# Optimization experiments

Measured on AMD Instinct MI355X. Metric: run time of the kernel, lower is better.

Reference implementation:

```python
import jax, jax.numpy as jnp
import numpy as np
from jax import lax

B, M = 8192, 200
OUT_W = OUT_H = 16
NUM_LAYERS = 32
CNN_CH = 64
FLAT = CNN_CH * 2 * 2  # conv5/s3: 16->4, conv3/s1: 4->2
INPUT_SIZE = 128
HIDDEN = 128
CRITIC_H = 1024
ACTOR_H = 512
EMB_D = 16
NUM_ACTIONS = 100


def setup_inputs() -> dict:
    key = jax.random.key(0)
    ks = jax.random.split(key, 20)
    # token observations: [coord_byte, attr_index, attr_value] packed as int32
    coords = jax.random.randint(ks[0], (B, M), 0, 256)          # coord byte; 255 = invalid token
    attrs = jax.random.randint(ks[1], (B, M), 0, 40)            # some >= NUM_LAYERS -> masked
    vals = jax.random.randint(ks[2], (B, M), 0, 256)
    observations = jnp.stack([coords, attrs, vals], axis=-1).astype(jnp.int32)

    def lin(k, out_d, in_d, scale=None):
        s = scale if scale is not None else 1.0 / np.sqrt(in_d)
        return jax.random.uniform(k, (out_d, in_d), jnp.float32, -s, s)

    max_vec = jax.random.uniform(ks[3], (1, NUM_LAYERS, 1, 1), jnp.float32, 0.5, 30.0)
    cnn1_w = jax.random.normal(ks[4], (CNN_CH, NUM_LAYERS, 5, 5), jnp.float32) * 0.05
    cnn1_b = jnp.zeros((CNN_CH,), jnp.float32)
    cnn2_w = jax.random.normal(ks[5], (CNN_CH, CNN_CH, 3, 3), jnp.float32) * 0.05
    cnn2_b = jnp.zeros((CNN_CH,), jnp.float32)
    fc1_w = lin(ks[6], 128, FLAT); fc1_b = jnp.zeros((128,), jnp.float32)
    enc_w = lin(ks[7], INPUT_SIZE, 128); enc_b = jnp.zeros((INPUT_SIZE,), jnp.float32)
    critic1_w = lin(ks[8], CRITIC_H, HIDDEN); critic1_b = jnp.zeros((CRITIC_H,), jnp.float32)
    value_w = lin(ks[9], 1, CRITIC_H); value_b = jnp.zeros((1,), jnp.float32)
    actor1_w = lin(ks[10], ACTOR_H, HIDDEN); actor1_b = jnp.zeros((ACTOR_H,), jnp.float32)
    emb = jax.random.normal(ks[11], (NUM_ACTIONS, EMB_D), jnp.float32)
    action_emb = emb * (0.1 / jnp.max(jnp.abs(emb)))
    bound = 1.0 / np.sqrt(ACTOR_H)
    actor_W = jax.random.uniform(ks[12], (1, ACTOR_H, EMB_D), jnp.float32, -bound, bound)
    actor_bias = jax.random.uniform(ks[13], (1,), jnp.float32, -bound, bound)
    return dict(observations=observations, max_vec=max_vec,
                cnn1_w=cnn1_w, cnn1_b=cnn1_b, cnn2_w=cnn2_w, cnn2_b=cnn2_b,
                fc1_w=fc1_w, fc1_b=fc1_b, enc_w=enc_w, enc_b=enc_b,
                critic1_w=critic1_w, critic1_b=critic1_b, value_w=value_w, value_b=value_b,
                actor1_w=actor1_w, actor1_b=actor1_b, action_emb=action_emb,
                actor_W=actor_W, actor_bias=actor_bias)


def _encode_box(observations):
    # bit-unpack coord byte, mask, scatter into dense [B, L, W, H] box
    coords = observations[..., 0]                       # [B, M]
    x_idx = (coords >> 4) & 15
    y_idx = coords & 15
    atr_idx = observations[..., 1]
    atr_val = observations[..., 2].astype(jnp.float32)
    valid = (coords != 255) & (atr_idx < NUM_LAYERS)
    dim = OUT_W * OUT_H
    combined = atr_idx * dim + x_idx * OUT_H + y_idx    # [B, M]
    safe_idx = jnp.where(valid, combined, 0)
    safe_val = jnp.where(valid, atr_val, 0.0)
    box = jnp.zeros((observations.shape[0], NUM_LAYERS * dim), jnp.float32)
    box = box.at[jnp.arange(observations.shape[0])[:, None], safe_idx].set(safe_val)
    return box.reshape(-1, NUM_LAYERS, OUT_W, OUT_H)


def _conv(x, w, b, stride):
    y = lax.conv_general_dilated(x, w, (stride, stride), 'VALID',
                                 dimension_numbers=('NCHW', 'OIHW', 'NCHW'))
    return y + b[None, :, None, None]


def reference(observations, max_vec, cnn1_w, cnn1_b, cnn2_w, cnn2_b, fc1_w, fc1_b,
              enc_w, enc_b, critic1_w, critic1_b, value_w, value_b,
              actor1_w, actor1_b, action_emb, actor_W, actor_bias):
    box = _encode_box(observations)
    x = box / max_vec
    x = jax.nn.relu(_conv(x, cnn1_w, cnn1_b, 3))
    x = jax.nn.relu(_conv(x, cnn2_w, cnn2_b, 1))
    x = x.reshape(x.shape[0], -1)                       # [B, FLAT]
    x = jax.nn.relu(x @ fc1_w.T + fc1_b)
    hidden = jax.nn.relu(x @ enc_w.T + enc_b)           # [B, 128]
    # critic
    cf = jnp.tanh(hidden @ critic1_w.T + critic1_b)
    value = cf @ value_w.T + value_b                    # [B, 1]
    # bilinear actor (k=1: query is action-independent)
    af = jax.nn.relu(hidden @ actor1_w.T + actor1_b)    # [B, ACTOR_H]
    query = jnp.tanh(jnp.einsum('bh,he->be', af, actor_W[0]))
    logits = query @ action_emb[:NUM_ACTIONS].T + actor_bias  # [B, NUM_ACTIONS]
    return logits, value
```

## Files before the change

kernel.cpp:

```cpp
#include <hip/hip_runtime.h>
#include <math.h>

#define B_ 8192

typedef __attribute__((ext_vector_type(8))) short short8;
typedef __attribute__((ext_vector_type(4))) float f32x4;

__device__ unsigned short g_w1p[51200];
__device__ unsigned short g_w2p[36864];
__device__ unsigned short g_fc1hi[32768], g_fc1lo[32768];
__device__ unsigned short g_enchi[16384], g_enclo[16384];
__device__ unsigned short g_crp[131072];
__device__ unsigned short g_acp[65536];
__device__ unsigned short g_qWp[8192];
__device__ unsigned short g_ACT1hi[8192*1024];

__device__ __forceinline__ unsigned short f2bf(float v){
    unsigned u = __builtin_bit_cast(unsigned, v);
    unsigned r = (u + 0x7fffu + ((u >> 16) & 1u)) >> 16;
    return (unsigned short)r;
}
__device__ __forceinline__ float bf2f(unsigned short h){
    unsigned u = ((unsigned)h) << 16;
    return __builtin_bit_cast(float, u);
}
__device__ __forceinline__ void split_store(float v, unsigned short* hi, unsigned short* lo){
    unsigned short h = f2bf(v);
    *hi = h;
    *lo = f2bf(v - bf2f(h));
}

__global__ __launch_bounds__(256) void prep_kernel(
    const float* __restrict__ w1, const float* __restrict__ maxv,
    const float* __restrict__ w2, const float* __restrict__ fc1,
    const float* __restrict__ enc, const float* __restrict__ cr,
    const float* __restrict__ ac, const float* __restrict__ aW)
{
    int d = blockIdx.x * 256 + threadIdx.x;
    if (d < 51200){
        int n = d / 800, k = d - n*800;
        int l = k / 25;
        float v = w1[d] / maxv[l];
        int kc = k >> 5, kh = k & 31, ng = n >> 4, r = n & 15;
        int idx = ((kc*4 + ng)*16 + r)*32 + kh;
        g_w1p[idx] = f2bf(v);
        return;
    }
    d -= 51200;
    if (d < 36864){
        int oc = d / 576, k2 = d - oc*576;
        int kxy = k2 >> 6, ic = k2 & 63;
        float v = w2[oc*576 + ic*9 + kxy];
        int kc = k2 >> 6, ks = (k2 >> 5) & 1, kq = k2 & 31, nt = oc >> 4, r = oc & 15;
        int idx = (((kc*2 + ks)*4 + nt)*16 + r)*32 + kq;
        g_w2p[idx] = f2bf(v);
        return;
    }
    d -= 36864;
    if (d < 32768){
        int n = d >> 8, kp = d & 255;
        float v = fc1[n*256 + (kp & 63)*4 + (kp >> 6)];
        int idx = ((((n >> 4)*8) + (kp >> 5))*16 + (n & 15))*32 + (kp & 31);
        split_store(v, &g_fc1hi[idx], &g_fc1lo[idx]);
        return;
    }
    d -= 32768;
    if (d < 16384){
        int n = d >> 7, k = d & 127;
        int idx = ((((n >> 4)*4) + (k >> 5))*16 + (n & 15))*32 + (k & 31);
        split_store(enc[d], &g_enchi[idx], &g_enclo[idx]);
        return;
    }
    d -= 16384;
    if (d < 131072){
        int n = d >> 7, k = d & 127;
        int idx = ((((n >> 4)*4) + (k >> 5))*16 + (n & 15))*32 + (k & 31);
        g_crp[idx] = f2bf(cr[d]);
        return;
    }
    d -= 131072;
    if (d < 65536){
        int n = d >> 7, k = d & 127;
        int idx = ((((n >> 4)*4) + (k >> 5))*16 + (n & 15))*32 + (k & 31);
        g_acp[idx] = f2bf(ac[d]);
        return;
    }
    d -= 65536;
    {
        int e = d >> 9, j = d & 511;
        int idx = ((j >> 5)*16 + e)*32 + (j & 31);
        g_qWp[idx] = f2bf(aW[j*16 + e]);
    }
}

#define APITCH2 424
__global__ __launch_bounds__(256, 5) void conv1_kernel(const int* __restrict__ obs,
                                                       const float* __restrict__ b1)
{
    const int b = blockIdx.x;
    const int tid = threadIdx.x;
    const int wave = tid >> 6, lane = tid & 63;
    const int l15 = lane & 15, lhi = lane >> 4;

    __shared__ int wtab[8192];
    unsigned short* sA = (unsigned short*)wtab;

    int   cells[2], xs[2], ys[2], ls[2];
    float vals[2];
    bool  valids[2], kept[2];
    #pragma unroll
    for (int u = 0; u < 2; u++){
        const int slot = tid + u*256;
        valids[u] = false; kept[u] = false; cells[u] = 0;
        if (slot < 400){
            const int si = (slot >= 200) ? 1 : 0;
            const int k  = slot - si*200;
            const int base = (b*2 + si)*600 + k*3;
            int coord = obs[base], atr = obs[base+1], val = obs[base+2];
            bool valid = (coord != 255) && (atr < 32);
            xs[u] = (coord >> 4) & 15;  ys[u] = coord & 15;  ls[u] = atr;
            cells[u] = valid ? (atr*256 + xs[u]*16 + ys[u]) : 0;
            vals[u]  = (float)val;
            valids[u] = valid;
        }
    }
    if (tid < 200) wtab[cells[0]] = -1;
    __syncthreads();
    if (tid < 200) atomicMax(&wtab[cells[0]], tid);
    __syncthreads();
    if (tid < 200) kept[0] = (wtab[cells[0]] == tid);
    __syncthreads();
    if (tid >= 200) wtab[cells[0]] = -1;
    if (tid < 144)  wtab[cells[1]] = -1;
    __syncthreads();
    if (tid >= 200) atomicMax(&wtab[cells[0]], tid - 200);
    if (tid < 144)  atomicMax(&wtab[cells[1]], tid + 56);
    __syncthreads();
    if (tid >= 200) kept[0] = (wtab[cells[0]] == tid - 200);
    if (tid < 144)  kept[1] = (wtab[cells[1]] == tid + 56);
    __syncthreads();

    f32x4 acc0e = {0,0,0,0}, acc1e = {0,0,0,0};
    f32x4 acc0o = {0,0,0,0}, acc1o = {0,0,0,0};
    const unsigned short* Bhp = &g_w1p[wave*512 + l15*32 + lhi*8];
    const unsigned short* A0 = &sA[l15*APITCH2 + lhi*8];
    const unsigned short* A1 = &sA[(16 + l15)*APITCH2 + lhi*8];

    #pragma unroll
    for (int pass = 0; pass < 2; pass++){
        for (int i = tid; i < 1696; i += 256)
            *(short8*)&sA[i * 8] = short8{0,0,0,0,0,0,0,0};
        __syncthreads();

        #pragma unroll
        for (int u = 0; u < 2; u++){
            const int slot = tid + u*256;
            if (slot < 400 && kept[u] && valids[u]){
                const int si = (slot >= 200) ? 1 : 0;
                const int x3 = xs[u]/3, rx = xs[u] - 3*x3;
                const int y3 = ys[u]/3, ry = ys[u] - 3*y3;
                const unsigned short hv = f2bf(vals[u]);
                #pragma unroll
                for (int d = 0; d < 4; d++){
                    const int dxd = d >> 1, dyd = d & 1;
                    const int ox = x3 - dxd, oy = y3 - dyd;
                    const int wx = rx + 3*dxd, wy = ry + 3*dyd;
                    if (((unsigned)ox <= 3u) && ((unsigned)oy <= 3u) && (wx < 5) && (wy < 5)){
                        const int c = ls[u]*25 + wx*5 + wy;
                        const bool inpass = (pass == 0) ? (c < 416) : (c >= 416);
                        if (inpass)
                            sA[(si*16 + ox*4 + oy)*APITCH2 + (c - pass*416)] = hv;
                    }
                }
            }
        }
        __syncthreads();

        const int kc0 = (pass == 0) ? 0 : 13;
        const int kc1 = (pass == 0) ? 13 : 25;
        #pragma unroll
        for (int kc = kc0; kc < kc1; kc++){
            const int kl = kc - kc0;
            short8 a0 = *(const short8*)&A0[kl*32];
            short8 a1 = *(const short8*)&A1[kl*32];
            const short8 bb8 = *(const short8*)&Bhp[kc*2048];
            if (kc & 1){
                acc0o = __builtin_amdgcn_mfma_f32_16x16x32_bf16(a0, bb8, acc0o, 0, 0, 0);
                acc1o = __builtin_amdgcn_mfma_f32_16x16x32_bf16(a1, bb8, acc1o, 0, 0, 0);
            } else {
                acc0e = __builtin_amdgcn_mfma_f32_16x16x32_bf16(a0, bb8, acc0e, 0, 0, 0);
                acc1e = __builtin_amdgcn_mfma_f32_16x16x32_bf16(a1, bb8, acc1e, 0, 0, 0);
            }
        }
        if (pass == 0) __syncthreads();
    }

    f32x4 acc0, acc1;
    #pragma unroll
    for (int j = 0; j < 4; j++){ acc0[j] = acc0e[j] + acc0o[j]; acc1[j] = acc1e[j] + acc1o[j]; }

    const int n = wave*16 + l15;
    const float bb = b1[n];
    #pragma unroll
    for (int j = 0; j < 4; j++){
        const int pos = lhi*4 + j;
        float v0 = fmaxf(acc0[j] + bb, 0.f);
        float v1 = fmaxf(acc1[j] + bb, 0.f);
        g_ACT1hi[(b*2    )*1024 + pos*64 + n] = f2bf(v0);
        g_ACT1hi[(b*2 + 1)*1024 + pos*64 + n] = f2bf(v1);
    }
}

__global__ __launch_bounds__(512, 4) void tail_kernel(
    const float* __restrict__ b2,   const float* __restrict__ fc1b,
    const float* __restrict__ encb, const float* __restrict__ crb,
    const float* __restrict__ vw,   const float* __restrict__ vb,
    const float* __restrict__ acb,  const float* __restrict__ emb,
    const float* __restrict__ abias, float* __restrict__ out)
{
    const int r0 = blockIdx.x * 16;
    const int tid = threadIdx.x, wave = tid >> 6, lane = tid & 63;
    const int l15 = lane & 15, lhi = lane >> 4;
    const int coff = l15*32 + lhi*8;

    __shared__ char smem[52736];
    unsigned short* sA1h = (unsigned short*)smem;
    unsigned short* sA1l = (unsigned short*)(smem + 8448);
    float*          qpart= (float*)smem;
    unsigned short* sXh  = (unsigned short*)(smem + 16896);
    unsigned short* sXl  = (unsigned short*)(smem + 21248);
    float* svred = (float*)(smem + 16896);
    float* sq    = (float*)(smem + 17408);
    float* semb  = (float*)(smem + 18496);
    unsigned short* sHh  = (unsigned short*)(smem + 25600);
    unsigned short* sHl  = (unsigned short*)(smem + 29952);
    unsigned short* cb   = (unsigned short*)(smem + 34304);
    unsigned short* sACT = (unsigned short*)(smem + 16896);

    {
        for (int u = tid; u < 2048; u += 512){
            const int row = u >> 7, c8 = (u & 127) * 8;
            *(short8*)&sACT[row*1032 + c8] = *(const short8*)&g_ACT1hi[(r0 + row)*1024 + c8];
        }
        __syncthreads();

        f32x4 c2acc[2] = {{0,0,0,0},{0,0,0,0}};
        const int tile0 = wave*2,     mt0 = tile0 >> 2, nt0 = tile0 & 3;
        const int tile1 = wave*2 + 1, mt1 = tile1 >> 2, nt1 = tile1 & 3;
        const int row0 = mt0*16 + l15, smp0 = row0 >> 2, px0 = (row0 >> 1) & 1, py0 = row0 & 1;
        const int row1 = mt1*16 + l15, smp1 = row1 >> 2, px1 = (row1 >> 1) & 1, py1 = row1 & 1;
        #pragma unroll
        for (int kc = 0; kc < 9; kc++){
            const int kx = kc / 3, ky = kc - 3*kx;
            const int cell0 = (px0 + kx)*4 + (py0 + ky);
            const int cell1 = (px1 + kx)*4 + (py1 + ky);
            #pragma unroll
            for (int ks = 0; ks < 2; ks++){
                const int kk = ks*32 + lhi*8;
                short8 a0 = *(const short8*)&sACT[smp0*1032 + cell0*64 + kk];
                short8 a1 = *(const short8*)&sACT[smp1*1032 + cell1*64 + kk];
                const short8 b0 = *(const short8*)&g_w2p[((kc*2 + ks)*4 + nt0)*512 + coff];
                const short8 b1 = *(const short8*)&g_w2p[((kc*2 + ks)*4 + nt1)*512 + coff];
                c2acc[0] = __builtin_amdgcn_mfma_f32_16x16x32_bf16(a0, b0, c2acc[0], 0, 0, 0);
                c2acc[1] = __builtin_amdgcn_mfma_f32_16x16x32_bf16(a1, b1, c2acc[1], 0, 0, 0);
            }
        }
        __syncthreads();
        #pragma unroll
        for (int wt = 0; wt < 2; wt++){
            const int tile = wave*2 + wt, mt = tile >> 2, nt = tile & 3;
            const int col = nt*16 + l15;
            const float bb = b2[col];
            #pragma unroll
            for (int j = 0; j < 4; j++){
                const int row = mt*16 + lhi*4 + j;
                float v = fmaxf(c2acc[wt][j] + bb, 0.f);
                unsigned short h = f2bf(v);
                const int ai = (row >> 2)*264 + (row & 3)*64 + col;
                sA1h[ai] = h;
                sA1l[ai] = f2bf(v - bf2f(h));
            }
        }
    }
    __syncthreads();

    {
        f32x4 acc = {0,0,0,0};
        const int n = wave*16 + l15;
        #pragma unroll
        for (int kk8 = 0; kk8 < 8; kk8++){
            const int kk = kk8*32 + lhi*8;
            short8 ah = *(const short8*)&sA1h[l15*264 + kk];
            short8 al = *(const short8*)&sA1l[l15*264 + kk];
            const short8 bh = *(const short8*)&g_fc1hi[(wave*8 + kk8)*512 + coff];
            const short8 bl = *(const short8*)&g_fc1lo[(wave*8 + kk8)*512 + coff];
            acc = __builtin_amdgcn_mfma_f32_16x16x32_bf16(ah, bh, acc, 0, 0, 0);
            acc = __builtin_amdgcn_mfma_f32_16x16x32_bf16(al, bh, acc, 0, 0, 0);
            acc = __builtin_amdgcn_mfma_f32_16x16x32_bf16(ah, bl, acc, 0, 0, 0);
        }
        __syncthreads();
        const float bb = fc1b[n];
        #pragma unroll
        for (int j = 0; j < 4; j++){
            const int row = lhi*4 + j;
            float v = fmaxf(acc[j] + bb, 0.f);
            unsigned short h = f2bf(v);
            sXh[row*136 + n] = h;
            sXl[row*136 + n] = f2bf(v - bf2f(h));
        }
    }
    __syncthreads();

    {
        f32x4 acc = {0,0,0,0};
        const int n = wave*16 + l15;
        #pragma unroll
        for (int kk4 = 0; kk4 < 4; kk4++){
            const int kk = kk4*32 + lhi*8;
            short8 ah = *(const short8*)&sXh[l15*136 + kk];
            short8 al = *(const short8*)&sXl[l15*136 + kk];
            const short8 bh = *(const short8*)&g_enchi[(wave*4 + kk4)*512 + coff];
            const short8 bl = *(const short8*)&g_enclo[(wave*4 + kk4)*512 + coff];
            acc = __builtin_amdgcn_mfma_f32_16x16x32_bf16(ah, bh, acc, 0, 0, 0);
            acc = __builtin_amdgcn_mfma_f32_16x16x32_bf16(al, bh, acc, 0, 0, 0);
            acc = __builtin_amdgcn_mfma_f32_16x16x32_bf16(ah, bl, acc, 0, 0, 0);
        }
        const float bb = encb[n];
        #pragma unroll
        for (int j = 0; j < 4; j++){
            const int row = lhi*4 + j;
            float v = fmaxf(acc[j] + bb, 0.f);
            unsigned short h = f2bf(v);
            sHh[row*136 + n] = h;
            sHl[row*136 + n] = f2bf(v - bf2f(h));
        }
    }
    __syncthreads();

    short8 Ah[4], Al[4];
    #pragma unroll
    for (int kk4 = 0; kk4 < 4; kk4++){
        const int kk = kk4*32 + lhi*8;
        Ah[kk4] = *(const short8*)&sHh[l15*136 + kk];
        Al[kk4] = *(const short8*)&sHl[l15*136 + kk];
    }

    {
        float vp[4] = {0,0,0,0};
        #pragma unroll
        for (int ntc = 0; ntc < 2; ntc++){
            f32x4 cacc[4];
            #pragma unroll
            for (int q = 0; q < 4; q++) cacc[q] = f32x4{0,0,0,0};
            #pragma unroll
            for (int q = 0; q < 4; q++){
                const int t = wave*8 + ntc*4 + q;
                #pragma unroll
                for (int kk4 = 0; kk4 < 4; kk4++){
                    const short8 bh = *(const short8*)&g_crp[(t*4 + kk4)*512 + coff];
                    cacc[q] = __builtin_amdgcn_mfma_f32_16x16x32_bf16(Ah[kk4], bh, cacc[q], 0, 0, 0);
                    cacc[q] = __builtin_amdgcn_mfma_f32_16x16x32_bf16(Al[kk4], bh, cacc[q], 0, 0, 0);
                }
            }
            #pragma unroll
            for (int q = 0; q < 4; q++){
                const int n = wave*128 + (ntc*4 + q)*16 + l15;
                const float w = vw[n], bb = crb[n];
                #pragma unroll
                for (int j = 0; j < 4; j++)
                    vp[j] += tanhf(cacc[q][j] + bb) * w;
            }
        }
        #pragma unroll
        for (int m = 1; m < 16; m <<= 1)
            #pragma unroll
            for (int j = 0; j < 4; j++) vp[j] += __shfl_xor(vp[j], m, 64);
        if (l15 == 0){
            #pragma unroll
            for (int j = 0; j < 4; j++)
                svred[wave*16 + lhi*4 + j] = vp[j];
        }
    }

    __syncthreads();
    f32x4 qacc = {0,0,0,0};
    {
        const int c = wave;
        f32x4 aacc[4];
        #pragma unroll
        for (int nt = 0; nt < 4; nt++) aacc[nt] = f32x4{0,0,0,0};
        #pragma unroll
        for (int kk4 = 0; kk4 < 4; kk4++){
            #pragma unroll
            for (int nt = 0; nt < 4; nt++){
                const int t = c*4 + nt;
                const short8 bh = *(const short8*)&g_acp[(t*4 + kk4)*512 + coff];
                aacc[nt] = __builtin_amdgcn_mfma_f32_16x16x32_bf16(Ah[kk4], bh, aacc[nt], 0, 0, 0);
                aacc[nt] = __builtin_amdgcn_mfma_f32_16x16x32_bf16(Al[kk4], bh, aacc[nt], 0, 0, 0);
            }
        }
        #pragma unroll
        for (int nt = 0; nt < 4; nt++){
            const int col = nt*16 + l15;
            const float bb = acb[c*64 + col];
            #pragma unroll
            for (int j = 0; j < 4; j++){
                const int row = lhi*4 + j;
                cb[(wave*16 + row)*72 + col] = f2bf(fmaxf(aacc[nt][j] + bb, 0.f));
            }
        }
        #pragma unroll
        for (int kk2 = 0; kk2 < 2; kk2++){
            const int kk = kk2*32 + lhi*8;
            const short8 qbh = *(const short8*)&g_qWp[(c*2 + kk2)*512 + coff];
            const short8 qah = *(const short8*)&cb[(wave*16 + l15)*72 + kk];
            qacc = __builtin_amdgcn_mfma_f32_16x16x32_bf16(qah, qbh, qacc, 0, 0, 0);
        }
    }
    #pragma unroll
    for (int j = 0; j < 4; j++)
        qpart[wave*256 + (lhi*4 + j)*16 + l15] = qacc[j];
    __syncthreads();

    if (tid < 16){
        float s = vb[0];
        #pragma unroll
        for (int w = 0; w < 8; w++) s += svred[w*16 + tid];
        out[B_*100 + r0 + tid] = s;
    }
    if (tid < 256){
        int row = tid >> 4, e = tid & 15;
        float s = 0.f;
        #pragma unroll
        for (int w = 0; w < 8; w++) s += qpart[w*256 + row*16 + e];
        sq[row*17 + e] = tanhf(s);
    }
    for (int k = tid; k < 1600; k += 512) semb[k] = emb[k];
    __syncthreads();
    for (int i = tid; i < 1600; i += 512){
        int row = i / 100, a = i - row*100;
        float s = abias[0];
        #pragma unroll
        for (int e = 0; e < 16; e++) s += sq[row*17 + e] * semb[a*16 + e];
        out[(r0 + row)*100 + a] = s;
    }
}

extern "C" void kernel_launch(void* const* d_in, const int* in_sizes, int n_in,
                              void* d_out, int out_size, void* d_ws, size_t ws_size,
                              hipStream_t stream) {
    const int*   obs   = (const int*)  d_in[0];
    const float* maxv  = (const float*)d_in[1];
    const float* w1    = (const float*)d_in[2];
    const float* b1    = (const float*)d_in[3];
    const float* w2    = (const float*)d_in[4];
    const float* b2    = (const float*)d_in[5];
    const float* fc1w  = (const float*)d_in[6];
    const float* fc1b  = (const float*)d_in[7];
    const float* encw  = (const float*)d_in[8];
    const float* encb  = (const float*)d_in[9];
    const float* crw   = (const float*)d_in[10];
    const float* crb   = (const float*)d_in[11];
    const float* vw    = (const float*)d_in[12];
    const float* vb    = (const float*)d_in[13];
    const float* acw   = (const float*)d_in[14];
    const float* acb   = (const float*)d_in[15];
    const float* emb   = (const float*)d_in[16];
    const float* aW    = (const float*)d_in[17];
    const float* abias = (const float*)d_in[18];
    float* out = (float*)d_out;

    prep_kernel<<<1336, 256, 0, stream>>>(w1, maxv, w2, fc1w, encw, crw, acw, aW);
    conv1_kernel<<<B_/2, 256, 0, stream>>>(obs, b1);
    tail_kernel<<<512, 512, 0, stream>>>(b2, fc1b, encb, crb, vw, vb, acb, emb, abias, out);
}
```

Measured before the change: 82.59 us.

## Process four samples per conv1 block to reuse weight loads across more MFMAs

Each conv1 block now handles four batch samples instead of two, so each B-fragment load of the conv weights feeds four MFMAs instead of two, and half as many blocks are launched. The dedup of tokens is serialised per sample over four rounds with barriers, the shared A tile doubles to 64 rows, and the even/odd accumulator split is dropped. Occupancy hint drops from 5 to 3 blocks per CU, and the extra barriers plus the larger zero-fill may offset the gain in weight reuse.

```diff
diff --git a/kernel.cpp b/kernel.cpp
--- a/kernel.cpp
+++ b/kernel.cpp
@@ -93,8 +93,8 @@
     }
 }
 
-#define APITCH2 424
-__global__ __launch_bounds__(256, 5) void conv1_kernel(const int* __restrict__ obs,
+#define APITCH4 424
+__global__ __launch_bounds__(256, 3) void conv1_kernel(const int* __restrict__ obs,
                                                        const float* __restrict__ b1)
 {
     const int b = blockIdx.x;
@@ -102,61 +102,58 @@
     const int wave = tid >> 6, lane = tid & 63;
     const int l15 = lane & 15, lhi = lane >> 4;
 
-    __shared__ int wtab[8192];
-    unsigned short* sA = (unsigned short*)wtab;
-
-    int   cells[2], xs[2], ys[2], ls[2];
-    float vals[2];
-    bool  valids[2], kept[2];
-    #pragma unroll
-    for (int u = 0; u < 2; u++){
+    __shared__ char smem[64 * APITCH4 * 2];
+    int* wtab = (int*)smem;
+    unsigned short* sA = (unsigned short*)smem;
+
+    int   cells[4], xs[4], ys[4], ls[4], ks[4], sis[4];
+    float vals[4];
+    bool  valids[4], kept[4], act[4];
+    #pragma unroll
+    for (int u = 0; u < 4; u++){
         const int slot = tid + u*256;
-        valids[u] = false; kept[u] = false; cells[u] = 0;
-        if (slot < 400){
-            const int si = (slot >= 200) ? 1 : 0;
+        act[u] = (slot < 800);
+        valids[u] = false; kept[u] = false; cells[u] = 0; sis[u] = 0; ks[u] = 0;
+        if (act[u]){
+            const int si = slot / 200;
             const int k  = slot - si*200;
-            const int base = (b*2 + si)*600 + k*3;
+            const int base = (b*4 + si)*600 + k*3;
             int coord = obs[base], atr = obs[base+1], val = obs[base+2];
             bool valid = (coord != 255) && (atr < 32);
             xs[u] = (coord >> 4) & 15;  ys[u] = coord & 15;  ls[u] = atr;
             cells[u] = valid ? (atr*256 + xs[u]*16 + ys[u]) : 0;
             vals[u]  = (float)val;
-            valids[u] = valid;
-        }
-    }
-    if (tid < 200) wtab[cells[0]] = -1;
-    __syncthreads();
-    if (tid < 200) atomicMax(&wtab[cells[0]], tid);
-    __syncthreads();
-    if (tid < 200) kept[0] = (wtab[cells[0]] == tid);
-    __syncthreads();
-    if (tid >= 200) wtab[cells[0]] = -1;
-    if (tid < 144)  wtab[cells[1]] = -1;
-    __syncthreads();
-    if (tid >= 200) atomicMax(&wtab[cells[0]], tid - 200);
-    if (tid < 144)  atomicMax(&wtab[cells[1]], tid + 56);
-    __syncthreads();
-    if (tid >= 200) kept[0] = (wtab[cells[0]] == tid - 200);
-    if (tid < 144)  kept[1] = (wtab[cells[1]] == tid + 56);
-    __syncthreads();
-
-    f32x4 acc0e = {0,0,0,0}, acc1e = {0,0,0,0};
-    f32x4 acc0o = {0,0,0,0}, acc1o = {0,0,0,0};
+            valids[u] = valid; sis[u] = si; ks[u] = k;
+        }
+    }
+    #pragma unroll
+    for (int s = 0; s < 4; s++){
+        #pragma unroll
+        for (int u = 0; u < 4; u++)
+            if (act[u] && sis[u] == s) wtab[cells[u]] = -1;
+        __syncthreads();
+        #pragma unroll
+        for (int u = 0; u < 4; u++)
+            if (act[u] && sis[u] == s) atomicMax(&wtab[cells[u]], ks[u]);
+        __syncthreads();
+        #pragma unroll
+        for (int u = 0; u < 4; u++)
+            if (act[u] && sis[u] == s) kept[u] = (wtab[cells[u]] == ks[u]);
+        __syncthreads();
+    }
+
+    f32x4 acc[4] = {{0,0,0,0},{0,0,0,0},{0,0,0,0},{0,0,0,0}};
     const unsigned short* Bhp = &g_w1p[wave*512 + l15*32 + lhi*8];
-    const unsigned short* A0 = &sA[l15*APITCH2 + lhi*8];
-    const unsigned short* A1 = &sA[(16 + l15)*APITCH2 + lhi*8];
 
     #pragma unroll
     for (int pass = 0; pass < 2; pass++){
-        for (int i = tid; i < 1696; i += 256)
+        for (int i = tid; i < 3392; i += 256)
             *(short8*)&sA[i * 8] = short8{0,0,0,0,0,0,0,0};
         __syncthreads();
 
         #pragma unroll
-        for (int u = 0; u < 2; u++){
-            const int slot = tid + u*256;
-            if (slot < 400 && kept[u] && valids[u]){
-                const int si = (slot >= 200) ? 1 : 0;
+        for (int u = 0; u < 4; u++){
+            if (act[u] && kept[u] && valids[u]){
                 const int x3 = xs[u]/3, rx = xs[u] - 3*x3;
                 const int y3 = ys[u]/3, ry = ys[u] - 3*y3;
                 const unsigned short hv = f2bf(vals[u]);
@@ -169,7 +166,7 @@
                         const int c = ls[u]*25 + wx*5 + wy;
                         const bool inpass = (pass == 0) ? (c < 416) : (c >= 416);
                         if (inpass)
-                            sA[(si*16 + ox*4 + oy)*APITCH2 + (c - pass*416)] = hv;
+                            sA[(sis[u]*16 + ox*4 + oy)*APITCH4 + (c - pass*416)] = hv;
                     }
                 }
             }
@@ -181,33 +178,26 @@
         #pragma unroll
         for (int kc = kc0; kc < kc1; kc++){
             const int kl = kc - kc0;
-            short8 a0 = *(const short8*)&A0[kl*32];
-            short8 a1 = *(const short8*)&A1[kl*32];
             const short8 bb8 = *(const short8*)&Bhp[kc*2048];
-            if (kc & 1){
-                acc0o = __builtin_amdgcn_mfma_f32_16x16x32_bf16(a0, bb8, acc0o, 0, 0, 0);
-                acc1o = __builtin_amdgcn_mfma_f32_16x16x32_bf16(a1, bb8, acc1o, 0, 0, 0);
-            } else {
-                acc0e = __builtin_amdgcn_mfma_f32_16x16x32_bf16(a0, bb8, acc0e, 0, 0, 0);
-                acc1e = __builtin_amdgcn_mfma_f32_16x16x32_bf16(a1, bb8, acc1e, 0, 0, 0);
+            #pragma unroll
+            for (int m = 0; m < 4; m++){
+                short8 am = *(const short8*)&sA[(m*16 + l15)*APITCH4 + kl*32 + lhi*8];
+                acc[m] = __builtin_amdgcn_mfma_f32_16x16x32_bf16(am, bb8, acc[m], 0, 0, 0);
             }
         }
         if (pass == 0) __syncthreads();
     }
-
-    f32x4 acc0, acc1;
-    #pragma unroll
-    for (int j = 0; j < 4; j++){ acc0[j] = acc0e[j] + acc0o[j]; acc1[j] = acc1e[j] + acc1o[j]; }
 
     const int n = wave*16 + l15;
     const float bb = b1[n];
     #pragma unroll
-    for (int j = 0; j < 4; j++){
-        const int pos = lhi*4 + j;
-        float v0 = fmaxf(acc0[j] + bb, 0.f);
-        float v1 = fmaxf(acc1[j] + bb, 0.f);
-        g_ACT1hi[(b*2    )*1024 + pos*64 + n] = f2bf(v0);
-        g_ACT1hi[(b*2 + 1)*1024 + pos*64 + n] = f2bf(v1);
+    for (int m = 0; m < 4; m++){
+        #pragma unroll
+        for (int j = 0; j < 4; j++){
+            const int pos = lhi*4 + j;
+            float v = fmaxf(acc[m][j] + bb, 0.f);
+            g_ACT1hi[(b*4 + m)*1024 + pos*64 + n] = f2bf(v);
+        }
     }
 }
 
@@ -471,6 +461,6 @@
     float* out = (float*)d_out;
 
     prep_kernel<<<1336, 256, 0, stream>>>(w1, maxv, w2, fc1w, encw, crw, acw, aW);
-    conv1_kernel<<<B_/2, 256, 0, stream>>>(obs, b1);
+    conv1_kernel<<<B_/4, 256, 0, stream>>>(obs, b1);
     tail_kernel<<<512, 512, 0, stream>>>(b2, fc1b, encb, crb, vw, vb, acb, emb, abias, out);
 }
```

Result: slower. 91.08 us (+10.3%).
